# Kernel tuning notes

Measured on AMD Instinct MI355X. Metric: run time of the kernel, lower is better.

Reference implementation:

```python
import jax, jax.numpy as jnp
import numpy as np

IN_CH, OUT_CH, KS = 64, 128, 3
GRID, DEG = 8, 3
STRIDE, PAD = 1, 1
SIZE = IN_CH * KS * KS            # 576
NCOEF = GRID + DEG                # 11
GRID_RANGE = (-1.0, 1.0)


def _xavier_uniform(key, shape):
    fan_out, fan_in = shape
    a = float(np.sqrt(6.0 / (fan_in + fan_out)))
    return jax.random.uniform(key, shape, minval=-a, maxval=a, dtype=jnp.float32)


def setup_inputs() -> dict:
    key = jax.random.key(0)
    k1, k2, k3 = jax.random.split(key, 3)
    x = jax.random.normal(k1, (8, IN_CH, 32, 32), dtype=jnp.float32)
    # non-trainable knot grid, one row per unfolded feature
    knots = jnp.tile(jnp.linspace(GRID_RANGE[0], GRID_RANGE[1], GRID + 1, dtype=jnp.float32)[None, :], (SIZE, 1))
    coeff = 0.1 * jax.random.normal(k2, (OUT_CH, SIZE, NCOEF), dtype=jnp.float32)
    base_weights = _xavier_uniform(k3, (OUT_CH, SIZE))
    spline_weights = jnp.ones((OUT_CH, SIZE), dtype=jnp.float32)
    return {"x": x, "knots": knots, "coeff": coeff,
            "base_weights": base_weights, "spline_weights": spline_weights}


def bspline_basis(x, grid, k):
    # x: (S, P) evaluation points; grid: (S, G+1) knots. Returns (S, G+k, P).
    h = (grid[:, -1:] - grid[:, :1]) / (grid.shape[1] - 1)
    left = grid[:, :1] - h * jnp.arange(k, 0, -1, dtype=x.dtype)
    right = grid[:, -1:] + h * jnp.arange(1, k + 1, dtype=x.dtype)
    g = jnp.concatenate([left, grid, right], axis=1)  # (S, G+1+2k)
    xe = x[:, None, :]
    B = ((xe >= g[:, :-1, None]) & (xe < g[:, 1:, None])).astype(x.dtype)
    for d in range(1, k + 1):  # de Boor recursion over fixed degree
        B = ((xe - g[:, :-(d + 1), None]) / (g[:, d:-1, None] - g[:, :-(d + 1), None]) * B[:, :-1]
             + (g[:, d + 1:, None] - xe) / (g[:, d + 1:, None] - g[:, 1:-d, None]) * B[:, 1:])
    return B


def _unfold(x):
    # torch F.unfold with channel-major (c, kh, kw) feature ordering
    N, C, H, W = x.shape
    xp = jnp.pad(x, ((0, 0), (0, 0), (PAD, PAD), (PAD, PAD)))
    Hp = (H + 2 * PAD - KS) // STRIDE + 1
    Wp = (W + 2 * PAD - KS) // STRIDE + 1
    patches = jnp.stack([xp[:, :, i:i + STRIDE * Hp:STRIDE, j:j + STRIDE * Wp:STRIDE]
                         for i in range(KS) for j in range(KS)], axis=2)  # (N, C, KS*KS, Hp, Wp)
    L = Hp * Wp
    u = patches.reshape(N, SIZE, L)              # (N, size, L)
    u = jnp.transpose(u, (1, 0, 2)).reshape(SIZE, N * L)  # (size, N*L), col = n*L + l
    return u, Hp, Wp


def reference(x, knots, coeff, base_weights, spline_weights):
    N = x.shape[0]
    u, Hp, Wp = _unfold(x)                                   # (size, P)
    base = base_weights @ jax.nn.silu(u)                     # (Cout, P)
    B = bspline_basis(u, knots, DEG)                         # (size, ncoef, P)
    eff = spline_weights[:, :, None] * coeff                 # (Cout, size, ncoef)
    spl = jnp.einsum('csj,sjp->cp', eff, B)                  # (Cout, P)
    out = (base + spl).reshape(OUT_CH, N, Hp, Wp)
    return jnp.transpose(out, (1, 0, 2, 3))                  # (N, Cout, Hp, Wp)
```

## Files before the change

### kernel.cpp

```cpp
#include <hip/hip_runtime.h>


typedef __attribute__((ext_vector_type(8))) short bf16x8;
typedef __attribute__((ext_vector_type(4))) float f32x4;
typedef __attribute__((ext_vector_type(4))) unsigned short u16x4;

#define WSWZ_BYTES 1769472
#define PART_OFF   WSWZ_BYTES

__device__ __forceinline__ short f2bf(float f) {
    union { float f; unsigned u; } c; c.f = f;
    unsigned r = c.u + 0x7fffu + ((c.u >> 16) & 1u);
    return (short)(r >> 16);
}
__device__ __forceinline__ float bf2f(unsigned short u) {
    union { unsigned u; float f; } c; c.u = ((unsigned)u) << 16;
    return c.f;
}

__global__ void kan_weights(const float* __restrict__ coeff,
                            const float* __restrict__ basew,
                            const float* __restrict__ splw,
                            short* __restrict__ Wswz) {
    __shared__ float coeffL[6336];
    __shared__ float basewL[576];
    __shared__ float splwL[576];
    const int co = blockIdx.x;
    const int t  = threadIdx.x;
    const float* crow = coeff + co * 6336;
    for (int i = t; i < 6336; i += 256) coeffL[i] = crow[i];
    for (int i = t; i < 576; i += 256) {
        basewL[i] = basew[co * 576 + i];
        splwL[i]  = splw[co * 576 + i];
    }
    __syncthreads();
    const int cb = co >> 4, lm = co & 15;
    for (int c = t; c < 864; c += 256) {
        int kk = c >> 2, quad = c & 3;
        int f  = kk / 18;
        int rm = kk - f * 18;
        int tap = rm >> 1, ks = rm & 1;
        bf16x8 pack;
#pragma unroll
        for (int j = 0; j < 8; ++j) {
            int ci = ks * 32 + quad * 8 + j;
            int s  = ci * 9 + tap;
            float v = (f == 0) ? basewL[s] : splwL[s] * coeffL[s * 11 + (f - 1)];
            pack[j] = f2bf(v);
        }
        *(bf16x8*)(Wswz + ((kk * 8 + cb) * 64 + quad * 16 + lm) * 8) = pack;
    }
}

__global__ __launch_bounds__(256, 2)
void kan_gemm(const float* __restrict__ x,
              const short* __restrict__ Wswz,
              float* __restrict__ part) {
    __shared__ unsigned short xs[4 * 64 * 36];
    __shared__ short Bs[3 * 8704];

    const int t    = threadIdx.x;
    const int w    = t >> 6;
    const int l    = t & 63;
    const int lp   = l & 15;
    const int quad = l >> 4;
    const int wm   = w >> 1;
    const int wn   = w & 1;

    const int bz    = blockIdx.x;
    const int fg    = bz & 3;
    const int ptile = bz >> 2;
    const int n     = ptile >> 4;
    const int y0    = (ptile & 15) << 1;

#pragma unroll
    for (int it = 0; it < 8; ++it) {
        int cg = t + it * 256;
        int rr = cg >> 9, ci = (cg >> 3) & 63, q = cg & 7;
        int y  = y0 - 1 + rr;
        f32x4 v = {0.f, 0.f, 0.f, 0.f};
        if (y >= 0 && y < 32)
            v = *(const f32x4*)(x + (((n * 64 + ci) * 32 + y) * 32 + q * 4));
        u16x4 p;
        p.x = (unsigned short)f2bf(v.x); p.y = (unsigned short)f2bf(v.y);
        p.z = (unsigned short)f2bf(v.z); p.w = (unsigned short)f2bf(v.w);
        *(u16x4*)&xs[(rr * 64 + ci) * 36 + q * 4] = p;
    }
    __syncthreads();

    const int f0 = fg * 3;
    for (int it = t; it < 1088; it += 256) {
        int rr  = it >> 8;
        int rem = it - rr * 272;
        rr  = it / 272;
        rem = it - rr * 272;
        int xp = rem >> 3, cch = rem & 7, c0 = cch << 3;
        bool interior = (xp >= 1 && xp <= 32);
        bf16x8 packs[3];
#pragma unroll
        for (int j = 0; j < 8; ++j) {
            float v = interior ? bf2f(xs[(rr * 64 + c0 + j) * 36 + (xp - 1)]) : 0.f;
            float sig  = 1.f / (1.f + expf(-v));
            float silu = v * sig;
            float tt = 4.f * v + 7.f;
            int   i0 = -100;
            float b0 = 0.f, b1 = 0.f, b2 = 0.f, b3 = 0.f;
            if (tt >= 0.f && tt < 14.f) {
                i0 = (int)tt;
                float fr  = tt - (float)i0;
                float omf = 1.f - fr;
                float fr2 = fr * fr, fr3 = fr2 * fr;
                b0 = omf * omf * omf * (1.f / 6.f);
                b1 = (3.f * fr3 - 6.f * fr2 + 4.f) * (1.f / 6.f);
                b2 = (-3.f * fr3 + 3.f * fr2 + 3.f * fr + 1.f) * (1.f / 6.f);
                b3 = fr3 * (1.f / 6.f);
            }
#pragma unroll
            for (int p = 0; p < 3; ++p) {
                int f = f0 + p;
                float val;
                if (f == 0) val = silu;
                else {
                    int jj = f - 1;
                    val = 0.f;
                    val = (jj == i0 - 3) ? b0 : val;
                    val = (jj == i0 - 2) ? b1 : val;
                    val = (jj == i0 - 1) ? b2 : val;
                    val = (jj == i0    ) ? b3 : val;
                }
                packs[p][j] = f2bf(val);
            }
        }
        int pix = rr * 34 + xp;
        int swz = (cch ^ (pix & 7)) << 3;
#pragma unroll
        for (int p = 0; p < 3; ++p)
            *(bf16x8*)&Bs[p * 8704 + pix * 64 + swz] = packs[p];
    }
    __syncthreads();

    f32x4 acc[4][2];
#pragma unroll
    for (int m = 0; m < 4; ++m)
#pragma unroll
        for (int nt = 0; nt < 2; ++nt) {
            f32x4 z = {0.f, 0.f, 0.f, 0.f};
            acc[m][nt] = z;
        }

#pragma unroll 1
    for (int p = 0; p < 3; ++p) {
        const short* B0 = Bs + p * 8704;
        const short* Af = Wswz + (long)((f0 + p) * 18) * 4096;
#pragma unroll
        for (int kk = 0; kk < 18; ++kk) {
            const int tap = kk >> 1, ks = kk & 1;
            const int dy  = tap / 3;
            const int dx  = tap - dy * 3;
            const short* Ak = Af + kk * 4096 + (wm * 4) * 512 + l * 8;
            bf16x8 a0 = *(const bf16x8*)(Ak);
            bf16x8 a1 = *(const bf16x8*)(Ak + 512);
            bf16x8 a2 = *(const bf16x8*)(Ak + 1024);
            bf16x8 a3 = *(const bf16x8*)(Ak + 1536);
            const int c = ks * 4 + quad;
#pragma unroll
            for (int nt = 0; nt < 2; ++nt) {
                int pix = (wn + dy) * 34 + (nt << 4) + lp + dx;
                bf16x8 b = *(const bf16x8*)&B0[pix * 64 + ((c ^ (pix & 7)) << 3)];
                acc[0][nt] = __builtin_amdgcn_mfma_f32_16x16x32_bf16(a0, b, acc[0][nt], 0, 0, 0);
                acc[1][nt] = __builtin_amdgcn_mfma_f32_16x16x32_bf16(a1, b, acc[1][nt], 0, 0, 0);
                acc[2][nt] = __builtin_amdgcn_mfma_f32_16x16x32_bf16(a2, b, acc[2][nt], 0, 0, 0);
                acc[3][nt] = __builtin_amdgcn_mfma_f32_16x16x32_bf16(a3, b, acc[3][nt], 0, 0, 0);
            }
        }
    }

    float* dst = part + (long)fg * 1048576;
#pragma unroll
    for (int m = 0; m < 4; ++m)
#pragma unroll
        for (int nt = 0; nt < 2; ++nt)
#pragma unroll
            for (int r = 0; r < 4; ++r) {
                int co = wm * 64 + m * 16 + quad * 4 + r;
                int y  = y0 + wn;
                int xx = (nt << 4) + lp;
                dst[((long)(n * 128 + co) * 32 + y) * 32 + xx] = acc[m][nt][r];
            }
}

__global__ void kan_reduce(const float* __restrict__ part,
                           float* __restrict__ out) {
    int g = blockIdx.x * 256 + threadIdx.x;
    f32x4 a = ((const f32x4*)part)[g];
#pragma unroll
    for (int s = 1; s < 4; ++s)
        a += ((const f32x4*)(part + (long)s * 1048576))[g];
    ((f32x4*)out)[g] = a;
}

extern "C" void kernel_launch(void* const* d_in, const int* in_sizes, int n_in,
                              void* d_out, int out_size, void* d_ws, size_t ws_size,
                              hipStream_t stream) {
    const float* x     = (const float*)d_in[0];
    const float* coeff = (const float*)d_in[2];
    const float* basew = (const float*)d_in[3];
    const float* splw  = (const float*)d_in[4];
    float* out = (float*)d_out;

    short* Wswz = (short*)d_ws;
    float* part = (float*)((char*)d_ws + PART_OFF);

    kan_weights<<<128, 256, 0, stream>>>(coeff, basew, splw, Wswz);
    kan_gemm<<<512, 256, 0, stream>>>(x, Wswz, part);
    kan_reduce<<<1024, 256, 0, stream>>>(part, out);
}
```

Before: 108.6 us.

## Restructure KAN GEMM with LDS-staged weights, split-K waves and double-buffered basis

Rearranges the GEMM so each 512-thread block covers 64 output channels and 8 rows, and splits the two K halves across waves with an LDS reduction at the end. Weights are staged into LDS through async global-to-LDS loads, and the per-feature B-spline basis tile is built into double-buffered LDS while the previous feature's MFMAs run. The aim is to cut redundant global weight loads and raise per-wave MFMA reuse with a 4x4 accumulator tile. In exchange the block uses more LDS and more registers, and the number of blocks halves.

```diff
diff --git a/kernel.cpp b/kernel.cpp
--- a/kernel.cpp
+++ b/kernel.cpp
@@ -3,7 +3,6 @@
 
 typedef __attribute__((ext_vector_type(8))) short bf16x8;
 typedef __attribute__((ext_vector_type(4))) float f32x4;
-typedef __attribute__((ext_vector_type(4))) unsigned short u16x4;
 
 #define WSWZ_BYTES 1769472
 #define PART_OFF   WSWZ_BYTES
@@ -13,9 +12,11 @@
     unsigned r = c.u + 0x7fffu + ((c.u >> 16) & 1u);
     return (short)(r >> 16);
 }
-__device__ __forceinline__ float bf2f(unsigned short u) {
-    union { unsigned u; float f; } c; c.u = ((unsigned)u) << 16;
-    return c.f;
+
+__device__ __forceinline__ void async16(const void* g, void* l) {
+    __builtin_amdgcn_global_load_lds(
+        (const __attribute__((address_space(1))) unsigned int*)g,
+        (__attribute__((address_space(3))) unsigned int*)l, 16, 0, 0);
 }
 
 __global__ void kan_weights(const float* __restrict__ coeff,
@@ -34,7 +35,9 @@
         splwL[i]  = splw[co * 576 + i];
     }
     __syncthreads();
-    const int cb = co >> 4, lm = co & 15;
+    const int cbh = co >> 6;
+    const int cb4 = (co >> 4) & 3;
+    const int lm  = co & 15;
     for (int c = t; c < 864; c += 256) {
         int kk = c >> 2, quad = c & 3;
         int f  = kk / 18;
@@ -48,79 +51,75 @@
             float v = (f == 0) ? basewL[s] : splwL[s] * coeffL[s * 11 + (f - 1)];
             pack[j] = f2bf(v);
         }
-        *(bf16x8*)(Wswz + ((kk * 8 + cb) * 64 + quad * 16 + lm) * 8) = pack;
-    }
-}
-
-__global__ __launch_bounds__(256, 2)
+        *(bf16x8*)(Wswz +
+            (size_t)(((((f * 2 + cbh) * 18 + rm) * 4 + cb4) * 64 + quad * 16 + lm)) * 8) = pack;
+    }
+}
+
+__global__ __launch_bounds__(512, 2)
 void kan_gemm(const float* __restrict__ x,
               const short* __restrict__ Wswz,
               float* __restrict__ part) {
-    __shared__ unsigned short xs[4 * 64 * 36];
-    __shared__ short Bs[3 * 8704];
+    __shared__ __align__(16) short Asl[36864];
+    __shared__ __align__(16) short Bsl[2][21760];
 
     const int t    = threadIdx.x;
     const int w    = t >> 6;
     const int l    = t & 63;
     const int lp   = l & 15;
     const int quad = l >> 4;
-    const int wm   = w >> 1;
-    const int wn   = w & 1;
-
-    const int bz    = blockIdx.x;
-    const int fg    = bz & 3;
-    const int ptile = bz >> 2;
-    const int n     = ptile >> 4;
-    const int y0    = (ptile & 15) << 1;
-
-#pragma unroll
-    for (int it = 0; it < 8; ++it) {
-        int cg = t + it * 256;
-        int rr = cg >> 9, ci = (cg >> 3) & 63, q = cg & 7;
-        int y  = y0 - 1 + rr;
-        f32x4 v = {0.f, 0.f, 0.f, 0.f};
-        if (y >= 0 && y < 32)
-            v = *(const f32x4*)(x + (((n * 64 + ci) * 32 + y) * 32 + q * 4));
-        u16x4 p;
-        p.x = (unsigned short)f2bf(v.x); p.y = (unsigned short)f2bf(v.y);
-        p.z = (unsigned short)f2bf(v.z); p.w = (unsigned short)f2bf(v.w);
-        *(u16x4*)&xs[(rr * 64 + ci) * 36 + q * 4] = p;
-    }
-    __syncthreads();
+    const int g    = w >> 1;
+    const int ks   = w & 1;
+
+    const int bz  = blockIdx.x;
+    const int fg  = bz & 3;
+    const int cbh = (bz >> 2) & 1;
+    const int idx = bz >> 3;
+    const int n   = idx >> 2;
+    const int y0  = (idx & 3) << 3;
 
     const int f0 = fg * 3;
-    for (int it = t; it < 1088; it += 256) {
-        int rr  = it >> 8;
-        int rem = it - rr * 272;
-        rr  = it / 272;
-        rem = it - rr * 272;
-        int xp = rem >> 3, cch = rem & 7, c0 = cch << 3;
-        bool interior = (xp >= 1 && xp <= 32);
-        bf16x8 packs[3];
-#pragma unroll
-        for (int j = 0; j < 8; ++j) {
-            float v = interior ? bf2f(xs[(rr * 64 + c0 + j) * 36 + (xp - 1)]) : 0.f;
-            float sig  = 1.f / (1.f + expf(-v));
-            float silu = v * sig;
-            float tt = 4.f * v + 7.f;
-            int   i0 = -100;
-            float b0 = 0.f, b1 = 0.f, b2 = 0.f, b3 = 0.f;
-            if (tt >= 0.f && tt < 14.f) {
-                i0 = (int)tt;
-                float fr  = tt - (float)i0;
-                float omf = 1.f - fr;
-                float fr2 = fr * fr, fr3 = fr2 * fr;
-                b0 = omf * omf * omf * (1.f / 6.f);
-                b1 = (3.f * fr3 - 6.f * fr2 + 4.f) * (1.f / 6.f);
-                b2 = (-3.f * fr3 + 3.f * fr2 + 3.f * fr + 1.f) * (1.f / 6.f);
-                b3 = fr3 * (1.f / 6.f);
-            }
-#pragma unroll
-            for (int p = 0; p < 3; ++p) {
-                int f = f0 + p;
+
+    auto stageA = [&](int f) {
+        const char* gsrc = (const char*)(Wswz + (size_t)(f * 2 + cbh) * 36864);
+        char* ldst = (char*)Asl;
+#pragma unroll
+        for (int it = 0; it < 9; ++it) {
+            int o = (it * 512 + t) * 16;
+            async16(gsrc + o, ldst + o);
+        }
+    };
+
+    auto buildB = [&](int f, int buf) {
+        short* B = Bsl[buf];
+        for (int it = t; it < 2720; it += 512) {
+            int rr  = it / 272;
+            int rem = it - rr * 272;
+            int xp  = rem >> 3, cch = rem & 7;
+            int y   = y0 - 1 + rr;
+            bool valid = (xp >= 1) & (xp <= 32) & (y >= 0) & (y < 32);
+            const float* xb = x + (((n * 64 + cch * 8) * 32 + y) * 32 + (xp - 1));
+            bf16x8 pack;
+#pragma unroll
+            for (int j = 0; j < 8; ++j) {
+                float v = valid ? xb[j * 1024] : 0.f;
                 float val;
-                if (f == 0) val = silu;
-                else {
+                if (f == 0) {
+                    val = v / (1.f + expf(-v));
+                } else {
+                    float tt = 4.f * v + 7.f;
+                    int   i0 = -100;
+                    float b0 = 0.f, b1 = 0.f, b2 = 0.f, b3 = 0.f;
+                    if (tt >= 0.f && tt < 14.f) {
+                        i0 = (int)tt;
+                        float fr  = tt - (float)i0;
+                        float omf = 1.f - fr;
+                        float fr2 = fr * fr, fr3 = fr2 * fr;
+                        b0 = omf * omf * omf * (1.f / 6.f);
+                        b1 = (3.f * fr3 - 6.f * fr2 + 4.f) * (1.f / 6.f);
+                        b2 = (-3.f * fr3 + 3.f * fr2 + 3.f * fr + 1.f) * (1.f / 6.f);
+                        b3 = fr3 * (1.f / 6.f);
+                    }
                     int jj = f - 1;
                     val = 0.f;
                     val = (jj == i0 - 3) ? b0 : val;
@@ -128,65 +127,82 @@
                     val = (jj == i0 - 1) ? b2 : val;
                     val = (jj == i0    ) ? b3 : val;
                 }
-                packs[p][j] = f2bf(val);
+                pack[j] = f2bf(val);
             }
-        }
-        int pix = rr * 34 + xp;
-        int swz = (cch ^ (pix & 7)) << 3;
-#pragma unroll
-        for (int p = 0; p < 3; ++p)
-            *(bf16x8*)&Bs[p * 8704 + pix * 64 + swz] = packs[p];
-    }
-    __syncthreads();
-
-    f32x4 acc[4][2];
+            int pix = rr * 34 + xp;
+            *(bf16x8*)&B[pix * 64 + ((cch ^ (pix & 7)) << 3)] = pack;
+        }
+    };
+
+    f32x4 acc[4][4];
 #pragma unroll
     for (int m = 0; m < 4; ++m)
 #pragma unroll
-        for (int nt = 0; nt < 2; ++nt) {
+        for (int nt = 0; nt < 4; ++nt) {
             f32x4 z = {0.f, 0.f, 0.f, 0.f};
             acc[m][nt] = z;
         }
 
+    stageA(f0);
+    buildB(f0, 0);
+    __syncthreads();
+
 #pragma unroll 1
     for (int p = 0; p < 3; ++p) {
-        const short* B0 = Bs + p * 8704;
-        const short* Af = Wswz + (long)((f0 + p) * 18) * 4096;
-#pragma unroll
-        for (int kk = 0; kk < 18; ++kk) {
-            const int tap = kk >> 1, ks = kk & 1;
-            const int dy  = tap / 3;
-            const int dx  = tap - dy * 3;
-            const short* Ak = Af + kk * 4096 + (wm * 4) * 512 + l * 8;
-            bf16x8 a0 = *(const bf16x8*)(Ak);
-            bf16x8 a1 = *(const bf16x8*)(Ak + 512);
-            bf16x8 a2 = *(const bf16x8*)(Ak + 1024);
-            bf16x8 a3 = *(const bf16x8*)(Ak + 1536);
-            const int c = ks * 4 + quad;
-#pragma unroll
-            for (int nt = 0; nt < 2; ++nt) {
-                int pix = (wn + dy) * 34 + (nt << 4) + lp + dx;
-                bf16x8 b = *(const bf16x8*)&B0[pix * 64 + ((c ^ (pix & 7)) << 3)];
-                acc[0][nt] = __builtin_amdgcn_mfma_f32_16x16x32_bf16(a0, b, acc[0][nt], 0, 0, 0);
-                acc[1][nt] = __builtin_amdgcn_mfma_f32_16x16x32_bf16(a1, b, acc[1][nt], 0, 0, 0);
-                acc[2][nt] = __builtin_amdgcn_mfma_f32_16x16x32_bf16(a2, b, acc[2][nt], 0, 0, 0);
-                acc[3][nt] = __builtin_amdgcn_mfma_f32_16x16x32_bf16(a3, b, acc[3][nt], 0, 0, 0);
+        if (p < 2) buildB(f0 + p + 1, (p + 1) & 1);
+
+        const short* B = Bsl[p & 1];
+#pragma unroll
+        for (int tap = 0; tap < 9; ++tap) {
+            const int kk = tap * 2 + ks;
+            const int dy = tap / 3;
+            const int dx = tap - dy * 3;
+            bf16x8 a[4], b[4];
+#pragma unroll
+            for (int m = 0; m < 4; ++m)
+                a[m] = *(const bf16x8*)&Asl[((kk * 4 + m) * 64 + l) * 8];
+            const int c0 = ks * 4 + quad;
+#pragma unroll
+            for (int nt = 0; nt < 4; ++nt) {
+                int pix = (2 * g + (nt >> 1) + dy) * 34 + ((nt & 1) << 4) + lp + dx;
+                b[nt] = *(const bf16x8*)&B[pix * 64 + ((c0 ^ (pix & 7)) << 3)];
             }
-        }
-    }
-
-    float* dst = part + (long)fg * 1048576;
-#pragma unroll
-    for (int m = 0; m < 4; ++m)
-#pragma unroll
-        for (int nt = 0; nt < 2; ++nt)
-#pragma unroll
-            for (int r = 0; r < 4; ++r) {
-                int co = wm * 64 + m * 16 + quad * 4 + r;
-                int y  = y0 + wn;
-                int xx = (nt << 4) + lp;
-                dst[((long)(n * 128 + co) * 32 + y) * 32 + xx] = acc[m][nt][r];
+#pragma unroll
+            for (int m = 0; m < 4; ++m)
+#pragma unroll
+                for (int nt = 0; nt < 4; ++nt)
+                    acc[m][nt] = __builtin_amdgcn_mfma_f32_16x16x32_bf16(a[m], b[nt], acc[m][nt], 0, 0, 0);
+        }
+        __syncthreads();
+        if (p < 2) stageA(f0 + p + 1);
+        __syncthreads();
+    }
+
+    float* red = (float*)Asl;
+    if (ks == 1) {
+#pragma unroll
+        for (int m = 0; m < 4; ++m)
+#pragma unroll
+            for (int nt = 0; nt < 4; ++nt)
+                *(f32x4*)&red[((g * 16 + m * 4 + nt) * 256 + l * 4)] = acc[m][nt];
+    }
+    __syncthreads();
+    if (ks == 0) {
+        float* dst = part + (size_t)fg * 1048576;
+#pragma unroll
+        for (int m = 0; m < 4; ++m)
+#pragma unroll
+            for (int nt = 0; nt < 4; ++nt) {
+                f32x4 o = acc[m][nt] + *(const f32x4*)&red[((g * 16 + m * 4 + nt) * 256 + l * 4)];
+                int y   = y0 + 2 * g + (nt >> 1);
+                int xxb = ((nt & 1) << 4) + lp;
+#pragma unroll
+                for (int r = 0; r < 4; ++r) {
+                    int co = cbh * 64 + m * 16 + quad * 4 + r;
+                    dst[((size_t)(n * 128 + co) * 32 + y) * 32 + xxb] = o[r];
+                }
             }
+    }
 }
 
 __global__ void kan_reduce(const float* __restrict__ part,
@@ -195,7 +211,7 @@
     f32x4 a = ((const f32x4*)part)[g];
 #pragma unroll
     for (int s = 1; s < 4; ++s)
-        a += ((const f32x4*)(part + (long)s * 1048576))[g];
+        a += ((const f32x4*)(part + (size_t)s * 1048576))[g];
     ((f32x4*)out)[g] = a;
 }
 
@@ -212,6 +228,6 @@
     float* part = (float*)((char*)d_ws + PART_OFF);
 
     kan_weights<<<128, 256, 0, stream>>>(coeff, basew, splw, Wswz);
-    kan_gemm<<<512, 256, 0, stream>>>(x, Wswz, part);
+    kan_gemm<<<256, 512, 0, stream>>>(x, Wswz, part);
     kan_reduce<<<1024, 256, 0, stream>>>(part, out);
 }
```

Measured after the change: 125.6 us. 15.6% more time.
